# Kernel tuning notes

Measured on AMD Instinct MI355X. Metric: run time of the kernel, lower is better.

## Reference

```python
import jax, jax.numpy as jnp
import numpy as np

EPS = 1e-12  # matches F.normalize eps

def _l2norm(x):
    n = jnp.sqrt(jnp.sum(x * x, axis=-1, keepdims=True))
    return x / jnp.maximum(n, EPS)

def setup_inputs() -> dict:
    key = jax.random.key(0)
    k1, k2, k3, k4 = jax.random.split(key, 4)
    Bq, Lq, H = 32, 32, 768
    ppq = 8
    Bd, Ld = Bq * ppq, 512
    dim = 128
    q_hidden = jax.random.normal(k1, (Bq, Lq, H), dtype=jnp.float32)
    d_hidden = jax.random.normal(k2, (Bd, Ld, H), dtype=jnp.float32)
    W = jax.random.normal(k3, (dim, H), dtype=jnp.float32) * (1.0 / np.sqrt(H))
    d_mask = jax.random.randint(k4, (Bd, Ld), 0, 2).astype(bool)
    d_mask = d_mask.at[:, 0].set(True)  # guarantee >=1 valid token per doc
    return {"q_hidden": q_hidden, "d_hidden": d_hidden, "W": W,
            "d_mask": d_mask, "ppq": ppq}

def reference(q_hidden, d_hidden, W, d_mask, ppq):
    # linear projection (no bias) + L2 normalize, as in query()/doc()
    q = _l2norm(jnp.einsum('bqh,dh->bqd', q_hidden, W))        # [Bq, Lq, dim]
    d = _l2norm(jnp.einsum('bkh,dh->bkd', d_hidden, W))        # [Bd, Ld, dim]
    d = d * d_mask[..., None].astype(d.dtype)                  # zero masked tokens
    qd = jnp.repeat(q, ppq, axis=0)                            # [Bd, Lq, dim]
    sim = jnp.einsum('bqd,bkd->bqk', qd, d)                    # cosine MaxSim scores
    sim = jnp.where(d_mask[:, None, :], sim, -jnp.inf)         # mask doc tokens
    return jnp.sum(jnp.max(sim, axis=-1), axis=-1)             # [Bd]
```

## Files before the change

kernel.cpp:

```cpp
#include <hip/hip_runtime.h>
#include <math.h>

#define H    768
#define NT   24
#define DIM  128
#define LQ   32
#define LD   512
#define BM   256
#define EPSF 1e-12f

typedef _Float16 f16x8 __attribute__((ext_vector_type(8)));
typedef _Float16 f16x4 __attribute__((ext_vector_type(4)));
typedef float    f32x4 __attribute__((ext_vector_type(4)));

static __device__ __forceinline__ unsigned short h2u(_Float16 h) {
    return __builtin_bit_cast(unsigned short, h);
}

#define GLOAD_LDS16(g, l) __builtin_amdgcn_global_load_lds(                    \
    (const __attribute__((address_space(1))) unsigned int*)(const void*)(g),   \
    (__attribute__((address_space(3))) unsigned int*)(void*)(l), 16, 0, 0)

__global__ __launch_bounds__(256) void wconv_kernel(
    const float* __restrict__ W, unsigned short* __restrict__ wsW)
{
    const int ks  = blockIdx.x;
    const int tid = threadIdx.x;
    #pragma unroll 4
    for (int i = 0; i < 16; ++i) {
        const int idx = tid + i * 256;
        const int row = idx >> 5, col = idx & 31;
        const float x = W[(size_t)row * H + ks * 32 + col];
        const _Float16 hi = (_Float16)x;
        const _Float16 lo = (_Float16)(x - (float)hi);
        const int colS = (((col >> 3) ^ ((row >> 1) & 3)) << 3) | (col & 7);
        wsW[(((size_t)ks * 2 + 0) * 128 + row) * 32 + colS] = h2u(hi);
        wsW[(((size_t)ks * 2 + 1) * 128 + row) * 32 + colS] = h2u(lo);
    }
}

__global__ __launch_bounds__(128) void qproj_kernel(
    const float* __restrict__ qh, const float* __restrict__ W,
    unsigned short* __restrict__ qn)
{
    const int blk = blockIdx.x;
    const int tid = threadIdx.x;
    __shared__ float rows[4][H];
    __shared__ float red[128];

    const float4* src = (const float4*)(qh + (size_t)blk * 4 * H);
    float4*       dst = (float4*)&rows[0][0];
    for (int i = tid; i < 4 * H / 4; i += 128) dst[i] = src[i];
    __syncthreads();

    const float4* w4 = (const float4*)(W + (size_t)tid * H);
    float acc[4] = {0.f, 0.f, 0.f, 0.f};
    for (int i = 0; i < H / 4; ++i) {
        float4 w = w4[i];
        #pragma unroll
        for (int j = 0; j < 4; ++j) {
            float4 x = ((const float4*)&rows[j][0])[i];
            acc[j] += w.x*x.x + w.y*x.y + w.z*x.z + w.w*x.w;
        }
    }
    #pragma unroll
    for (int j = 0; j < 4; ++j) {
        red[tid] = acc[j] * acc[j];
        __syncthreads();
        for (int s = 64; s > 0; s >>= 1) {
            if (tid < s) red[tid] += red[tid + s];
            __syncthreads();
        }
        const float inv = 1.0f / fmaxf(sqrtf(red[0]), EPSF);
        qn[((size_t)blk * 4 + j) * DIM + tid] = h2u((_Float16)(acc[j] * inv));
        __syncthreads();
    }
}

struct Smem {
    union {
        struct {
            unsigned short A[2][BM][32];
            unsigned short Wt[2][2][128][32];
        } g;
        unsigned short C[BM][DIM];
    } u;
    float         pnorm[2][BM];
    unsigned char mk[BM];
    float         pmax[LQ][8];
};

__global__ __launch_bounds__(512, 4) void docgemm_kernel(
    const float* __restrict__ dh, const unsigned short* __restrict__ wsW,
    const int* __restrict__ dmask, const unsigned short* __restrict__ qn,
    float* __restrict__ part, const int* __restrict__ ppq_p)
{
    __shared__ Smem sm;
    const int blk = blockIdx.x;
    const int b   = blk >> 1;
    const int c   = blk & 1;
    const int tid = threadIdx.x;
    const int w   = tid >> 6;
    const int wm  = w >> 1, wn = w & 1;
    const int l   = tid & 63;
    const int g   = l >> 4;
    const int r15 = l & 15;
    const int ppq = ppq_p[0];

    const int r0   = tid >> 3;
    const int seg0 = tid & 7;
    const int aswz = (r0 >> 1) & 3;
    const int coli = (((seg0 >> 1) ^ aswz) << 3) | ((seg0 & 1) << 2);

    const float* Abase = dh + ((size_t)b * LD + (size_t)c * BM) * H;

    f32x4 acc[4][4];
    #pragma unroll
    for (int m = 0; m < 4; ++m)
        #pragma unroll
        for (int n = 0; n < 4; ++n)
            acc[m][n] = (f32x4){0.f, 0.f, 0.f, 0.f};

    float4 avA[4];

    {
        const char* wt   = (const char*)wsW;
        char*       wdst = (char*)&sm.u.g.Wt[0][0][0][0];
        GLOAD_LDS16(wt + tid * 16,        wdst + (w * 64) * 16);
        GLOAD_LDS16(wt + 8192 + tid * 16, wdst + 8192 + (w * 64) * 16);
        __builtin_amdgcn_sched_barrier(0);
        #pragma unroll
        for (int i = 0; i < 4; ++i)
            avA[i] = *(const float4*)(Abase + (size_t)(r0 + i * 64) * H + seg0 * 4);
        #pragma unroll
        for (int i = 0; i < 4; ++i) {
            const int row = r0 + i * 64;
            f16x4 h;
            h[0] = (_Float16)avA[i].x; h[1] = (_Float16)avA[i].y;
            h[2] = (_Float16)avA[i].z; h[3] = (_Float16)avA[i].w;
            *(f16x4*)&sm.u.g.A[0][row][coli] = h;
        }
        #pragma unroll
        for (int i = 0; i < 4; ++i)
            avA[i] = *(const float4*)(Abase + (size_t)(r0 + i * 64) * H + 32 + seg0 * 4);
        asm volatile("s_waitcnt vmcnt(4) lgkmcnt(0)" ::: "memory");
        __builtin_amdgcn_sched_barrier(0);
        __builtin_amdgcn_s_barrier();
        __builtin_amdgcn_sched_barrier(0);
    }

    for (int t = 0; t < NT; ++t) {
        const int cur = t & 1, nxt = cur ^ 1;

        if (t + 1 < NT) {
            const char* wt   = (const char*)wsW + (size_t)(t + 1) * 16384;
            char*       wdst = (char*)&sm.u.g.Wt[nxt][0][0][0];
            GLOAD_LDS16(wt + tid * 16,        wdst + (w * 64) * 16);
            GLOAD_LDS16(wt + 8192 + tid * 16, wdst + 8192 + (w * 64) * 16);
        }
        __builtin_amdgcn_sched_barrier(0);

        f16x8 ah[4];
        #pragma unroll
        for (int m = 0; m < 4; ++m) {
            const int row = wm * 64 + m * 16 + r15;
            const int sl  = (g ^ ((row >> 1) & 3)) * 8;
            ah[m] = *(const f16x8*)&sm.u.g.A[cur][row][sl];
        }
        __builtin_amdgcn_s_setprio(1);
        #pragma unroll
        for (int n = 0; n < 4; ++n) {
            const int row = wn * 64 + n * 16 + r15;
            const int sl  = (g ^ ((row >> 1) & 3)) * 8;
            f16x8 bh = *(const f16x8*)&sm.u.g.Wt[cur][0][row][sl];
            f16x8 bl = *(const f16x8*)&sm.u.g.Wt[cur][1][row][sl];
            #pragma unroll
            for (int m = 0; m < 4; ++m)
                acc[m][n] = __builtin_amdgcn_mfma_f32_16x16x32_f16(ah[m], bh, acc[m][n], 0, 0, 0);
            #pragma unroll
            for (int m = 0; m < 4; ++m)
                acc[m][n] = __builtin_amdgcn_mfma_f32_16x16x32_f16(ah[m], bl, acc[m][n], 0, 0, 0);
        }
        __builtin_amdgcn_s_setprio(0);

        if (t + 1 < NT) {
            #pragma unroll
            for (int i = 0; i < 4; ++i) {
                const int row = r0 + i * 64;
                f16x4 h;
                h[0] = (_Float16)avA[i].x; h[1] = (_Float16)avA[i].y;
                h[2] = (_Float16)avA[i].z; h[3] = (_Float16)avA[i].w;
                *(f16x4*)&sm.u.g.A[nxt][row][coli] = h;
            }
        }
        if (t + 2 < NT) {
            const int k0n = (t + 2) * 32;
            #pragma unroll
            for (int i = 0; i < 4; ++i)
                avA[i] = *(const float4*)(Abase + (size_t)(r0 + i * 64) * H + k0n + seg0 * 4);
        }

        if (t + 2 < NT) {
            asm volatile("s_waitcnt vmcnt(4) lgkmcnt(0)" ::: "memory");
        } else {
            asm volatile("s_waitcnt vmcnt(0) lgkmcnt(0)" ::: "memory");
        }
        __builtin_amdgcn_sched_barrier(0);
        __builtin_amdgcn_s_barrier();
        __builtin_amdgcn_sched_barrier(0);
    }

    #pragma unroll
    for (int m = 0; m < 4; ++m) {
        const int tokb = wm * 64 + m * 16 + g * 4;
        #pragma unroll
        for (int n = 0; n < 4; ++n) {
            const int dim = wn * 64 + n * 16 + r15;
            #pragma unroll
            for (int r = 0; r < 4; ++r) {
                const int tok  = tokb + r;
                const int slot = (dim >> 3) ^ (tok & 7);
                sm.u.C[tok][slot * 8 + (dim & 7)] = h2u((_Float16)acc[m][n][r]);
            }
        }
    }
    #pragma unroll
    for (int m = 0; m < 4; ++m) {
        #pragma unroll
        for (int r = 0; r < 4; ++r) {
            float s = 0.f;
            #pragma unroll
            for (int n = 0; n < 4; ++n) s += acc[m][n][r] * acc[m][n][r];
            s += __shfl_xor(s, 1); s += __shfl_xor(s, 2);
            s += __shfl_xor(s, 4); s += __shfl_xor(s, 8);
            if (r15 == 0) sm.pnorm[wn][wm * 64 + m * 16 + g * 4 + r] = s;
        }
    }
    if (tid < BM) sm.mk[tid] = (unsigned char)(dmask[(size_t)b * LD + c * BM + tid] != 0);
    __syncthreads();

    const unsigned short* qb = qn + (size_t)(b / ppq) * LQ * DIM;
    const int t0 = w * 32 + r15, t1 = t0 + 16;
    const float inv0 = 1.0f / fmaxf(sqrtf(sm.pnorm[0][t0] + sm.pnorm[1][t0]), EPSF);
    const float inv1 = 1.0f / fmaxf(sqrtf(sm.pnorm[0][t1] + sm.pnorm[1][t1]), EPSF);

    f32x4 sacc[2][2];
    #pragma unroll
    for (int m = 0; m < 2; ++m)
        #pragma unroll
        for (int n = 0; n < 2; ++n)
            sacc[m][n] = (f32x4){0.f, 0.f, 0.f, 0.f};
    #pragma unroll
    for (int ks = 0; ks < 4; ++ks) {
        f16x8 qa[2], cb[2];
        #pragma unroll
        for (int m = 0; m < 2; ++m)
            qa[m] = *(const f16x8*)(qb + (size_t)(m * 16 + r15) * DIM + ks * 32 + g * 8);
        #pragma unroll
        for (int n = 0; n < 2; ++n) {
            const int row  = w * 32 + n * 16 + r15;
            const int slot = (ks * 4 + g) ^ (row & 7);
            cb[n] = *(const f16x8*)&sm.u.C[row][slot * 8];
        }
        #pragma unroll
        for (int m = 0; m < 2; ++m)
            #pragma unroll
            for (int n = 0; n < 2; ++n)
                sacc[m][n] = __builtin_amdgcn_mfma_f32_16x16x32_f16(qa[m], cb[n], sacc[m][n], 0, 0, 0);
    }

    const int m0 = sm.mk[t0], m1 = sm.mk[t1];
    #pragma unroll
    for (int m = 0; m < 2; ++m) {
        #pragma unroll
        for (int r = 0; r < 4; ++r) {
            float v0 = m0 ? sacc[m][0][r] * inv0 : -INFINITY;
            float v1 = m1 ? sacc[m][1][r] * inv1 : -INFINITY;
            float vmax = fmaxf(v0, v1);
            vmax = fmaxf(vmax, __shfl_xor(vmax, 1));
            vmax = fmaxf(vmax, __shfl_xor(vmax, 2));
            vmax = fmaxf(vmax, __shfl_xor(vmax, 4));
            vmax = fmaxf(vmax, __shfl_xor(vmax, 8));
            if (r15 == 0) sm.pmax[m * 16 + g * 4 + r][w] = vmax;
        }
    }
    __syncthreads();
    if (tid < LQ) {
        float mv = sm.pmax[tid][0];
        #pragma unroll
        for (int j = 1; j < 8; ++j) mv = fmaxf(mv, sm.pmax[tid][j]);
        part[(size_t)blk * 32 + tid] = mv;
    }
}

__global__ __launch_bounds__(64) void final_kernel(
    const float* __restrict__ part, float* __restrict__ out)
{
    const int b = blockIdx.x;
    const int q = threadIdx.x & 31;
    const float* p = part + (size_t)b * 64;
    float m = fmaxf(p[q], p[32 + q]);
    #pragma unroll
    for (int off = 1; off < 32; off <<= 1) m += __shfl_xor(m, off);
    if (threadIdx.x == 0) out[b] = m;
}

extern "C" void kernel_launch(void* const* d_in, const int* in_sizes, int n_in,
                              void* d_out, int out_size, void* d_ws, size_t ws_size,
                              hipStream_t stream) {
    const float* qh    = (const float*)d_in[0];
    const float* dh    = (const float*)d_in[1];
    const float* W     = (const float*)d_in[2];
    const int*   dmask = (const int*)d_in[3];
    const int*   ppq   = (const int*)d_in[4];
    float*       out   = (float*)d_out;

    unsigned short* wsW  = (unsigned short*)d_ws;
    unsigned short* qn   = (unsigned short*)((char*)d_ws + 393216);
    float*          part = (float*)((char*)d_ws + 393216 + 262144);

    const int nq = in_sizes[0] / H;
    const int Bd = out_size;

    wconv_kernel<<<NT, 256, 0, stream>>>(W, wsW);
    qproj_kernel<<<nq / 4, 128, 0, stream>>>(qh, W, qn);
    docgemm_kernel<<<Bd * 2, 512, 0, stream>>>(dh, wsW, dmask, qn, part, ppq);
    final_kernel<<<Bd, 64, 0, stream>>>(part, out);
}
```

Before: 144.2 us.

## Load GEMM operands directly from global into registers, drop LDS staging

The doc GEMM main loop no longer stages A and W tiles through double-buffered LDS with barriers. Each lane now loads its fp32 A fragment straight from global memory, converts it to fp16 in registers, and reads W fragments from global memory, so all per-tile LDS traffic and block-wide syncs disappear. The cost is that loads are issued with no software prefetch, so global latency is exposed on each iteration. W is also no longer shared across waves through LDS, which raises cache traffic. Separately, the q projection now reads a transposed fp32 copy of W that wconv writes, giving coalesced per-thread loads.

```diff
diff --git a/kernel.cpp b/kernel.cpp
--- a/kernel.cpp
+++ b/kernel.cpp
@@ -10,19 +10,15 @@
 #define EPSF 1e-12f
 
 typedef _Float16 f16x8 __attribute__((ext_vector_type(8)));
-typedef _Float16 f16x4 __attribute__((ext_vector_type(4)));
 typedef float    f32x4 __attribute__((ext_vector_type(4)));
 
 static __device__ __forceinline__ unsigned short h2u(_Float16 h) {
     return __builtin_bit_cast(unsigned short, h);
 }
 
-#define GLOAD_LDS16(g, l) __builtin_amdgcn_global_load_lds(                    \
-    (const __attribute__((address_space(1))) unsigned int*)(const void*)(g),   \
-    (__attribute__((address_space(3))) unsigned int*)(void*)(l), 16, 0, 0)
-
 __global__ __launch_bounds__(256) void wconv_kernel(
-    const float* __restrict__ W, unsigned short* __restrict__ wsW)
+    const float* __restrict__ W, unsigned short* __restrict__ wsW,
+    float* __restrict__ WT)
 {
     const int ks  = blockIdx.x;
     const int tid = threadIdx.x;
@@ -33,14 +29,14 @@
         const float x = W[(size_t)row * H + ks * 32 + col];
         const _Float16 hi = (_Float16)x;
         const _Float16 lo = (_Float16)(x - (float)hi);
-        const int colS = (((col >> 3) ^ ((row >> 1) & 3)) << 3) | (col & 7);
-        wsW[(((size_t)ks * 2 + 0) * 128 + row) * 32 + colS] = h2u(hi);
-        wsW[(((size_t)ks * 2 + 1) * 128 + row) * 32 + colS] = h2u(lo);
+        wsW[(((size_t)ks * 2 + 0) * 128 + row) * 32 + col] = h2u(hi);
+        wsW[(((size_t)ks * 2 + 1) * 128 + row) * 32 + col] = h2u(lo);
+        WT[((size_t)ks * 32 + col) * DIM + row] = x;
     }
 }
 
 __global__ __launch_bounds__(128) void qproj_kernel(
-    const float* __restrict__ qh, const float* __restrict__ W,
+    const float* __restrict__ qh, const float* __restrict__ WT,
     unsigned short* __restrict__ qn)
 {
     const int blk = blockIdx.x;
@@ -53,15 +49,14 @@
     for (int i = tid; i < 4 * H / 4; i += 128) dst[i] = src[i];
     __syncthreads();
 
-    const float4* w4 = (const float4*)(W + (size_t)tid * H);
     float acc[4] = {0.f, 0.f, 0.f, 0.f};
-    for (int i = 0; i < H / 4; ++i) {
-        float4 w = w4[i];
-        #pragma unroll
-        for (int j = 0; j < 4; ++j) {
-            float4 x = ((const float4*)&rows[j][0])[i];
-            acc[j] += w.x*x.x + w.y*x.y + w.z*x.z + w.w*x.w;
-        }
+    #pragma unroll 8
+    for (int h = 0; h < H; ++h) {
+        const float wv = WT[(size_t)h * DIM + tid];
+        acc[0] += wv * rows[0][h];
+        acc[1] += wv * rows[1][h];
+        acc[2] += wv * rows[2][h];
+        acc[3] += wv * rows[3][h];
     }
     #pragma unroll
     for (int j = 0; j < 4; ++j) {
@@ -78,16 +73,10 @@
 }
 
 struct Smem {
-    union {
-        struct {
-            unsigned short A[2][BM][32];
-            unsigned short Wt[2][2][128][32];
-        } g;
-        unsigned short C[BM][DIM];
-    } u;
-    float         pnorm[2][BM];
-    unsigned char mk[BM];
-    float         pmax[LQ][8];
+    unsigned short C[BM][DIM];
+    float          pnorm[2][BM];
+    unsigned char  mk[BM];
+    float          pmax[LQ][8];
 };
 
 __global__ __launch_bounds__(512, 4) void docgemm_kernel(
@@ -107,12 +96,9 @@
     const int r15 = l & 15;
     const int ppq = ppq_p[0];
 
-    const int r0   = tid >> 3;
-    const int seg0 = tid & 7;
-    const int aswz = (r0 >> 1) & 3;
-    const int coli = (((seg0 >> 1) ^ aswz) << 3) | ((seg0 & 1) << 2);
-
-    const float* Abase = dh + ((size_t)b * LD + (size_t)c * BM) * H;
+    const float* Abase =
+        dh + ((size_t)b * LD + c * BM + wm * 64 + r15) * H + g * 8;
+    const unsigned short* Wlane = wsW + (wn * 64 + r15) * 32 + g * 8;
 
     f32x4 acc[4][4];
     #pragma unroll
@@ -121,93 +107,36 @@
         for (int n = 0; n < 4; ++n)
             acc[m][n] = (f32x4){0.f, 0.f, 0.f, 0.f};
 
-    float4 avA[4];
-
-    {
-        const char* wt   = (const char*)wsW;
-        char*       wdst = (char*)&sm.u.g.Wt[0][0][0][0];
-        GLOAD_LDS16(wt + tid * 16,        wdst + (w * 64) * 16);
-        GLOAD_LDS16(wt + 8192 + tid * 16, wdst + 8192 + (w * 64) * 16);
-        __builtin_amdgcn_sched_barrier(0);
-        #pragma unroll
-        for (int i = 0; i < 4; ++i)
-            avA[i] = *(const float4*)(Abase + (size_t)(r0 + i * 64) * H + seg0 * 4);
-        #pragma unroll
-        for (int i = 0; i < 4; ++i) {
-            const int row = r0 + i * 64;
-            f16x4 h;
-            h[0] = (_Float16)avA[i].x; h[1] = (_Float16)avA[i].y;
-            h[2] = (_Float16)avA[i].z; h[3] = (_Float16)avA[i].w;
-            *(f16x4*)&sm.u.g.A[0][row][coli] = h;
-        }
-        #pragma unroll
-        for (int i = 0; i < 4; ++i)
-            avA[i] = *(const float4*)(Abase + (size_t)(r0 + i * 64) * H + 32 + seg0 * 4);
-        asm volatile("s_waitcnt vmcnt(4) lgkmcnt(0)" ::: "memory");
-        __builtin_amdgcn_sched_barrier(0);
-        __builtin_amdgcn_s_barrier();
-        __builtin_amdgcn_sched_barrier(0);
-    }
-
     for (int t = 0; t < NT; ++t) {
-        const int cur = t & 1, nxt = cur ^ 1;
-
-        if (t + 1 < NT) {
-            const char* wt   = (const char*)wsW + (size_t)(t + 1) * 16384;
-            char*       wdst = (char*)&sm.u.g.Wt[nxt][0][0][0];
-            GLOAD_LDS16(wt + tid * 16,        wdst + (w * 64) * 16);
-            GLOAD_LDS16(wt + 8192 + tid * 16, wdst + 8192 + (w * 64) * 16);
-        }
-        __builtin_amdgcn_sched_barrier(0);
-
-        f16x8 ah[4];
+        float4 a0[4], a1[4];
         #pragma unroll
         for (int m = 0; m < 4; ++m) {
-            const int row = wm * 64 + m * 16 + r15;
-            const int sl  = (g ^ ((row >> 1) & 3)) * 8;
-            ah[m] = *(const f16x8*)&sm.u.g.A[cur][row][sl];
-        }
+            const float4* p = (const float4*)(Abase + (size_t)m * 16 * H + t * 32);
+            a0[m] = p[0];
+            a1[m] = p[1];
+        }
+        f16x8 af[4];
+        #pragma unroll
+        for (int m = 0; m < 4; ++m) {
+            af[m][0] = (_Float16)a0[m].x; af[m][1] = (_Float16)a0[m].y;
+            af[m][2] = (_Float16)a0[m].z; af[m][3] = (_Float16)a0[m].w;
+            af[m][4] = (_Float16)a1[m].x; af[m][5] = (_Float16)a1[m].y;
+            af[m][6] = (_Float16)a1[m].z; af[m][7] = (_Float16)a1[m].w;
+        }
+        const unsigned short* wt = Wlane + (size_t)t * 8192;
         __builtin_amdgcn_s_setprio(1);
         #pragma unroll
         for (int n = 0; n < 4; ++n) {
-            const int row = wn * 64 + n * 16 + r15;
-            const int sl  = (g ^ ((row >> 1) & 3)) * 8;
-            f16x8 bh = *(const f16x8*)&sm.u.g.Wt[cur][0][row][sl];
-            f16x8 bl = *(const f16x8*)&sm.u.g.Wt[cur][1][row][sl];
+            f16x8 bh = *(const f16x8*)(wt + n * 512);
+            f16x8 bl = *(const f16x8*)(wt + 4096 + n * 512);
             #pragma unroll
             for (int m = 0; m < 4; ++m)
-                acc[m][n] = __builtin_amdgcn_mfma_f32_16x16x32_f16(ah[m], bh, acc[m][n], 0, 0, 0);
+                acc[m][n] = __builtin_amdgcn_mfma_f32_16x16x32_f16(af[m], bh, acc[m][n], 0, 0, 0);
             #pragma unroll
             for (int m = 0; m < 4; ++m)
-                acc[m][n] = __builtin_amdgcn_mfma_f32_16x16x32_f16(ah[m], bl, acc[m][n], 0, 0, 0);
+                acc[m][n] = __builtin_amdgcn_mfma_f32_16x16x32_f16(af[m], bl, acc[m][n], 0, 0, 0);
         }
         __builtin_amdgcn_s_setprio(0);
-
-        if (t + 1 < NT) {
-            #pragma unroll
-            for (int i = 0; i < 4; ++i) {
-                const int row = r0 + i * 64;
-                f16x4 h;
-                h[0] = (_Float16)avA[i].x; h[1] = (_Float16)avA[i].y;
-                h[2] = (_Float16)avA[i].z; h[3] = (_Float16)avA[i].w;
-                *(f16x4*)&sm.u.g.A[nxt][row][coli] = h;
-            }
-        }
-        if (t + 2 < NT) {
-            const int k0n = (t + 2) * 32;
-            #pragma unroll
-            for (int i = 0; i < 4; ++i)
-                avA[i] = *(const float4*)(Abase + (size_t)(r0 + i * 64) * H + k0n + seg0 * 4);
-        }
-
-        if (t + 2 < NT) {
-            asm volatile("s_waitcnt vmcnt(4) lgkmcnt(0)" ::: "memory");
-        } else {
-            asm volatile("s_waitcnt vmcnt(0) lgkmcnt(0)" ::: "memory");
-        }
-        __builtin_amdgcn_sched_barrier(0);
-        __builtin_amdgcn_s_barrier();
-        __builtin_amdgcn_sched_barrier(0);
     }
 
     #pragma unroll
@@ -220,7 +149,7 @@
             for (int r = 0; r < 4; ++r) {
                 const int tok  = tokb + r;
                 const int slot = (dim >> 3) ^ (tok & 7);
-                sm.u.C[tok][slot * 8 + (dim & 7)] = h2u((_Float16)acc[m][n][r]);
+                sm.C[tok][slot * 8 + (dim & 7)] = h2u((_Float16)acc[m][n][r]);
             }
         }
     }
@@ -260,7 +189,7 @@
         for (int n = 0; n < 2; ++n) {
             const int row  = w * 32 + n * 16 + r15;
             const int slot = (ks * 4 + g) ^ (row & 7);
-            cb[n] = *(const f16x8*)&sm.u.C[row][slot * 8];
+            cb[n] = *(const f16x8*)&sm.C[row][slot * 8];
         }
         #pragma unroll
         for (int m = 0; m < 2; ++m)
@@ -316,14 +245,15 @@
     float*       out   = (float*)d_out;
 
     unsigned short* wsW  = (unsigned short*)d_ws;
-    unsigned short* qn   = (unsigned short*)((char*)d_ws + 393216);
-    float*          part = (float*)((char*)d_ws + 393216 + 262144);
+    float*          WT   = (float*)((char*)d_ws + 393216);
+    unsigned short* qn   = (unsigned short*)((char*)d_ws + 786432);
+    float*          part = (float*)((char*)d_ws + 1048576);
 
     const int nq = in_sizes[0] / H;
     const int Bd = out_size;
 
-    wconv_kernel<<<NT, 256, 0, stream>>>(W, wsW);
-    qproj_kernel<<<nq / 4, 128, 0, stream>>>(qh, W, qn);
+    wconv_kernel<<<NT, 256, 0, stream>>>(W, wsW, WT);
+    qproj_kernel<<<nq / 4, 128, 0, stream>>>(qh, WT, qn);
     docgemm_kernel<<<Bd * 2, 512, 0, stream>>>(dh, wsW, dmask, qn, part, ppq);
     final_kernel<<<Bd, 64, 0, stream>>>(part, out);
 }
```

New measurement: 193.3 us. 34.0% more time.
